# Kernel tuning notes

Measured on AMD Instinct MI355X. Metric: run time of the kernel, lower is better.

The kernel has to match this reference:

```python
import jax, jax.numpy as jnp
import numpy as np

B, S, H = 1, 1024, 1024   # batch, seq, hidden_size
E, I = 8, 2048            # num_local_experts, intermediate_size
JITTER_EPS = 0.01         # config.router_jitter_noise


def setup_inputs() -> dict:
    key = jax.random.key(0)
    ks = jax.random.split(key, 5)
    s_h = 1.0 / np.sqrt(H)
    s_i = 1.0 / np.sqrt(I)
    return {
        "hidden_states": jax.random.normal(ks[0], (B, S, H), jnp.float32),
        "gate_w": jax.random.normal(ks[1], (E, H), jnp.float32) * s_h,   # nn.Linear(H, E) weight
        "w1": jax.random.normal(ks[2], (E, I, H), jnp.float32) * s_h,    # per-expert Linear(H, I)
        "w2": jax.random.normal(ks[3], (E, H, I), jnp.float32) * s_i,    # per-expert Linear(I, H)
        "w3": jax.random.normal(ks[4], (E, I, H), jnp.float32) * s_h,    # per-expert Linear(H, I)
    }


def _sparse_mixer_top2(scores, jitter_eps):
    # masked_sampling_omp_inference (top_k=2, inference)
    vals, idx = jax.lax.top_k(scores, 2)                 # [T,2]
    neg_inf = jnp.array(-jnp.inf, scores.dtype)

    t1 = vals[:, :1]                                      # top-1 logit
    f1 = jnp.maximum(jnp.abs(scores), t1)                 # clamp(min=t1)
    m1 = (t1 - scores) / f1 > 2 * jitter_eps
    p1 = jax.nn.softmax(jnp.where(m1, neg_inf, scores), axis=-1)
    mult1 = jnp.take_along_axis(p1, idx[:, :1], axis=-1)

    t2 = vals[:, 1:2]                                     # top-2 logit
    f2 = jnp.maximum(jnp.abs(scores), t2)
    m2 = (t2 - scores) / f2 > 2 * jitter_eps
    rows = jnp.arange(scores.shape[0])[:, None]
    s2 = scores.at[rows, idx[:, :1]].set(neg_inf)         # scatter -inf at top-1 slot
    p2 = jax.nn.softmax(jnp.where(m2, neg_inf, s2), axis=-1)
    mult2 = jnp.take_along_axis(p2, idx[:, 1:2], axis=-1)

    return jnp.concatenate([mult1, mult2], axis=-1), idx  # [T,2], [T,2]


def reference(hidden_states, gate_w, w1, w2, w3):
    b, s, h = hidden_states.shape
    x = hidden_states.reshape(-1, h)                      # [T,H]
    T = x.shape[0]

    logits = x @ gate_w.T                                 # [T,E] router logits
    mult, sel = _sparse_mixer_top2(logits, JITTER_EPS)

    # dense [T,E] combine weights (zero for unselected experts);
    # mathematically identical to gather/expert-FFN/scatter-add with full capacity
    rows = jnp.arange(T)[:, None]
    dense_w = jnp.zeros((T, E), x.dtype).at[rows, sel].set(mult)

    h1 = jnp.einsum('th,eih->eti', x, w1)                 # [E,T,I]
    h3 = jnp.einsum('th,eih->eti', x, w3)                 # [E,T,I]
    act = jax.nn.silu(h1) * h3                            # SwiGLU
    y = jnp.einsum('eti,ehi->eth', act, w2)               # [E,T,H]
    out = jnp.einsum('eth,te->th', y, dense_w)            # weighted combine
    return out.reshape(b, s, h)
```

## Files before the change

kernel.cpp:

```cpp
#include <hip/hip_runtime.h>
#include <hip/hip_bf16.h>
#include <math.h>

#define TT 1024
#define HD 1024
#define NE 8
#define ID 2048
#define MAXSLOT 3072
constexpr float JEPS = 0.01f;

typedef __attribute__((ext_vector_type(8))) short bf16x8;
typedef __attribute__((ext_vector_type(4))) float f32x4;

__device__ __forceinline__ float silu_f(float v) {
    return v / (1.f + expf(-v));
}

__device__ __forceinline__ unsigned short f2bf(float f) {
    unsigned int u = __float_as_uint(f);
    u += 0x7FFF + ((u >> 16) & 1);
    return (unsigned short)(u >> 16);
}

__device__ __forceinline__ void st_bf4(unsigned short* p, float4 v) {
    __hip_bfloat162 lo = __float22bfloat162_rn(make_float2(v.x, v.y));
    __hip_bfloat162 hi = __float22bfloat162_rn(make_float2(v.z, v.w));
    union { __hip_bfloat162 h[2]; uint2 q; } pk;
    pk.h[0] = lo; pk.h[1] = hi;
    *(uint2*)p = pk.q;
}

__global__ __launch_bounds__(256) void gate_kernel(
    const float* __restrict__ x, const float* __restrict__ gw,
    int* __restrict__ sel, float* __restrict__ wgt, int* __restrict__ counts,
    unsigned short* __restrict__ xbf)
{
    int wave = threadIdx.x >> 6;
    int lane = threadIdx.x & 63;
    int t = blockIdx.x * 4 + wave;

    const float4* x4 = (const float4*)(x + (size_t)t * HD);
    const float4* g4 = (const float4*)gw;

    float acc[8] = {0.f,0.f,0.f,0.f,0.f,0.f,0.f,0.f};
    #pragma unroll
    for (int c = 0; c < 4; ++c) {
        float4 xv = x4[lane + c * 64];
        st_bf4(&xbf[(size_t)t * HD + (size_t)(lane + c * 64) * 4], xv);
        #pragma unroll
        for (int e = 0; e < 8; ++e) {
            float4 gv = g4[e * 256 + lane + c * 64];
            acc[e] += xv.x*gv.x + xv.y*gv.y + xv.z*gv.z + xv.w*gv.w;
        }
    }
    #pragma unroll
    for (int e = 0; e < 8; ++e) {
        float v = acc[e];
        #pragma unroll
        for (int off = 32; off > 0; off >>= 1) v += __shfl_xor(v, off, 64);
        acc[e] = v;
    }

    if (lane == 0) {
        float s[8];
        #pragma unroll
        for (int e = 0; e < 8; ++e) s[e] = acc[e];

        int i0 = 0; float t1 = s[0];
        #pragma unroll
        for (int e = 1; e < 8; ++e) { if (s[e] > t1) { t1 = s[e]; i0 = e; } }
        int i1 = -1; float t2 = -INFINITY;
        #pragma unroll
        for (int e = 0; e < 8; ++e) {
            if (e == i0) continue;
            if (s[e] > t2) { t2 = s[e]; i1 = e; }
        }

        float sum1 = 0.f;
        #pragma unroll
        for (int e = 0; e < 8; ++e) {
            if (e == i0) { sum1 += 1.f; continue; }
            float f = fmaxf(fabsf(s[e]), t1);
            bool masked = (t1 - s[e]) > 2.f * JEPS * f;
            if (!masked) sum1 += expf(s[e] - t1);
        }
        float w0 = 1.f / sum1;

        float sum2 = 0.f;
        #pragma unroll
        for (int e = 0; e < 8; ++e) {
            if (e == i0) continue;
            if (e == i1) { sum2 += 1.f; continue; }
            float f = fmaxf(fabsf(s[e]), t2);
            bool masked = (t2 - s[e]) > 2.f * JEPS * f;
            if (!masked) sum2 += expf(s[e] - t2);
        }
        float w1v = 1.f / sum2;

        sel[t * 2 + 0] = i0; sel[t * 2 + 1] = i1;
        wgt[t * 2 + 0] = w0; wgt[t * 2 + 1] = w1v;
        atomicAdd(&counts[i0], 1);
        atomicAdd(&counts[i1], 1);
    }
}

__global__ void offsets_kernel(const int* __restrict__ counts,
                               int* __restrict__ offs, int* __restrict__ cursor)
{
    int o = 0;
    for (int e = 0; e < NE; ++e) {
        offs[e] = o;
        cursor[e] = o;
        o += (counts[e] + 127) & ~127;
    }
}

__global__ __launch_bounds__(256) void scatter_kernel(
    const int* __restrict__ sel, const float* __restrict__ wgt,
    int* __restrict__ cursor, int* __restrict__ slot_token,
    float* __restrict__ slot_weight)
{
    int t = blockIdx.x * 256 + threadIdx.x;
    #pragma unroll
    for (int j = 0; j < 2; ++j) {
        int e = sel[t * 2 + j];
        int pos = atomicAdd(&cursor[e], 1);
        slot_token[pos] = t;
        slot_weight[pos] = wgt[t * 2 + j];
    }
}

__global__ __launch_bounds__(256) void ffn1_kernel(
    const unsigned short* __restrict__ xbf, const float* __restrict__ w1,
    const float* __restrict__ w3, const int* __restrict__ counts,
    const int* __restrict__ offs, const int* __restrict__ slot_token,
    unsigned short* __restrict__ act)
{
    int bid = blockIdx.x;
    int e = bid & 7;
    int r = bid >> 3;
    int it = r & 31, tt = r >> 5;
    int cnt = counts[e];
    if (tt * 128 >= cnt) return;
    int base = offs[e];

    __shared__ unsigned short Xs[2][128][40];
    __shared__ unsigned short W1s[2][64][40];
    __shared__ unsigned short W3s[2][64][40];

    int t = threadIdx.x;
    int xr = t >> 1, xs = (t & 1) * 16;
    int srow = tt * 128 + xr;
    int tok = (srow < cnt) ? slot_token[base + srow] : slot_token[base];
    const unsigned short* xptr = xbf + (size_t)tok * HD;
    int wrow = t >> 2, ws0 = t & 3;
    const float* w1ptr = w1 + ((size_t)e * ID + (size_t)it * 64 + wrow) * HD;
    const float* w3ptr = w3 + ((size_t)e * ID + (size_t)it * 64 + wrow) * HD;

    int wid = t >> 6, lane = t & 63;
    int wr = wid >> 1, wc = wid & 1;
    int fr = lane & 15, fg = lane >> 4;

    f32x4 a1[4][2], a3[4][2];
    #pragma unroll
    for (int m = 0; m < 4; ++m)
        #pragma unroll
        for (int n = 0; n < 2; ++n) {
            a1[m][n] = (f32x4){0.f, 0.f, 0.f, 0.f};
            a3[m][n] = (f32x4){0.f, 0.f, 0.f, 0.f};
        }

    uint4 pxa0, pxb0, pxa1, pxb1;
    float4 pw10[2], pw30[2], pw11[2], pw31[2];

#define F1_LOAD0(KT) do { \
    pxa0 = *(const uint4*)(xptr + (KT) + xs); \
    pxb0 = *(const uint4*)(xptr + (KT) + xs + 8); \
    pw10[0] = *(const float4*)(w1ptr + (KT) + ws0 * 4); \
    pw10[1] = *(const float4*)(w1ptr + (KT) + (ws0 + 4) * 4); \
    pw30[0] = *(const float4*)(w3ptr + (KT) + ws0 * 4); \
    pw30[1] = *(const float4*)(w3ptr + (KT) + (ws0 + 4) * 4); \
} while (0)
#define F1_LOAD1(KT) do { \
    pxa1 = *(const uint4*)(xptr + (KT) + xs); \
    pxb1 = *(const uint4*)(xptr + (KT) + xs + 8); \
    pw11[0] = *(const float4*)(w1ptr + (KT) + ws0 * 4); \
    pw11[1] = *(const float4*)(w1ptr + (KT) + (ws0 + 4) * 4); \
    pw31[0] = *(const float4*)(w3ptr + (KT) + ws0 * 4); \
    pw31[1] = *(const float4*)(w3ptr + (KT) + (ws0 + 4) * 4); \
} while (0)
#define F1_STORE0(B) do { \
    *(uint4*)&Xs[B][xr][xs] = pxa0; \
    *(uint4*)&Xs[B][xr][xs + 8] = pxb0; \
    st_bf4(&W1s[B][wrow][ws0 * 4], pw10[0]); \
    st_bf4(&W1s[B][wrow][(ws0 + 4) * 4], pw10[1]); \
    st_bf4(&W3s[B][wrow][ws0 * 4], pw30[0]); \
    st_bf4(&W3s[B][wrow][(ws0 + 4) * 4], pw30[1]); \
} while (0)
#define F1_STORE1(B) do { \
    *(uint4*)&Xs[B][xr][xs] = pxa1; \
    *(uint4*)&Xs[B][xr][xs + 8] = pxb1; \
    st_bf4(&W1s[B][wrow][ws0 * 4], pw11[0]); \
    st_bf4(&W1s[B][wrow][(ws0 + 4) * 4], pw11[1]); \
    st_bf4(&W3s[B][wrow][ws0 * 4], pw31[0]); \
    st_bf4(&W3s[B][wrow][(ws0 + 4) * 4], pw31[1]); \
} while (0)
#define F1_COMPUTE(B) do { \
    bf16x8 af[4], b1f[2], b3f[2]; \
    _Pragma("unroll") for (int m = 0; m < 4; ++m) \
        af[m] = *(const bf16x8*)&Xs[B][wr * 64 + m * 16 + fr][fg * 8]; \
    _Pragma("unroll") for (int n = 0; n < 2; ++n) { \
        b1f[n] = *(const bf16x8*)&W1s[B][wc * 32 + n * 16 + fr][fg * 8]; \
        b3f[n] = *(const bf16x8*)&W3s[B][wc * 32 + n * 16 + fr][fg * 8]; } \
    _Pragma("unroll") for (int m = 0; m < 4; ++m) \
        _Pragma("unroll") for (int n = 0; n < 2; ++n) { \
            a1[m][n] = __builtin_amdgcn_mfma_f32_16x16x32_bf16(af[m], b1f[n], a1[m][n], 0, 0, 0); \
            a3[m][n] = __builtin_amdgcn_mfma_f32_16x16x32_bf16(af[m], b3f[n], a3[m][n], 0, 0, 0); } \
} while (0)

    F1_LOAD0(0);
    F1_LOAD1(32);
    F1_STORE0(0);

    for (int kt = 0; kt < HD; kt += 64) {
        __syncthreads();
        if (kt + 64 < HD) F1_LOAD0(kt + 64);
        F1_COMPUTE(0);
        F1_STORE1(1);
        __syncthreads();
        if (kt + 96 < HD) F1_LOAD1(kt + 96);
        F1_COMPUTE(1);
        if (kt + 64 < HD) F1_STORE0(0);
    }
#undef F1_LOAD0
#undef F1_LOAD1
#undef F1_STORE0
#undef F1_STORE1
#undef F1_COMPUTE

    size_t rowbase = (size_t)(base + tt * 128);
    #pragma unroll
    for (int m = 0; m < 4; ++m)
        #pragma unroll
        for (int n = 0; n < 2; ++n)
            #pragma unroll
            for (int rr = 0; rr < 4; ++rr) {
                int lrow = wr * 64 + m * 16 + fg * 4 + rr;
                int col  = it * 64 + wc * 32 + n * 16 + fr;
                float v = silu_f(a1[m][n][rr]) * a3[m][n][rr];
                act[(rowbase + lrow) * ID + col] = f2bf(v);
            }
}

__global__ __launch_bounds__(256) void ffn2_kernel(
    const unsigned short* __restrict__ act, const float* __restrict__ w2,
    const int* __restrict__ counts, const int* __restrict__ offs,
    const int* __restrict__ slot_token, const float* __restrict__ slot_weight,
    float* __restrict__ out)
{
    int bid = blockIdx.x;
    int e = bid & 7;
    int r = bid >> 3;
    int ht = r & 15, tt = r >> 4;
    int cnt = counts[e];
    if (tt * 128 >= cnt) return;
    int base = offs[e];

    __shared__ unsigned short As[2][128][40];
    __shared__ unsigned short Bs[2][64][40];

    int t = threadIdx.x;
    int ar = t >> 1, as = (t & 1) * 16;
    const unsigned short* aptr = act + (size_t)(base + tt * 128 + ar) * ID;
    int wrow = t >> 2, ws0 = t & 3;
    const float* w2ptr = w2 + ((size_t)e * HD + (size_t)ht * 64 + wrow) * ID;

    int wid = t >> 6, lane = t & 63;
    int wr = wid >> 1, wc = wid & 1;
    int fr = lane & 15, fg = lane >> 4;

    f32x4 acc[4][2];
    #pragma unroll
    for (int m = 0; m < 4; ++m)
        #pragma unroll
        for (int n = 0; n < 2; ++n) acc[m][n] = (f32x4){0.f, 0.f, 0.f, 0.f};

    uint4 pa00, pa01, pa10, pa11;
    float4 pb0[2], pb1[2];

#define F2_LOAD0(KT) do { \
    pa00 = *(const uint4*)(aptr + (KT) + as); \
    pa01 = *(const uint4*)(aptr + (KT) + as + 8); \
    pb0[0] = *(const float4*)(w2ptr + (KT) + ws0 * 4); \
    pb0[1] = *(const float4*)(w2ptr + (KT) + (ws0 + 4) * 4); \
} while (0)
#define F2_LOAD1(KT) do { \
    pa10 = *(const uint4*)(aptr + (KT) + as); \
    pa11 = *(const uint4*)(aptr + (KT) + as + 8); \
    pb1[0] = *(const float4*)(w2ptr + (KT) + ws0 * 4); \
    pb1[1] = *(const float4*)(w2ptr + (KT) + (ws0 + 4) * 4); \
} while (0)
#define F2_STORE0(B) do { \
    *(uint4*)&As[B][ar][as] = pa00; \
    *(uint4*)&As[B][ar][as + 8] = pa01; \
    st_bf4(&Bs[B][wrow][ws0 * 4], pb0[0]); \
    st_bf4(&Bs[B][wrow][(ws0 + 4) * 4], pb0[1]); \
} while (0)
#define F2_STORE1(B) do { \
    *(uint4*)&As[B][ar][as] = pa10; \
    *(uint4*)&As[B][ar][as + 8] = pa11; \
    st_bf4(&Bs[B][wrow][ws0 * 4], pb1[0]); \
    st_bf4(&Bs[B][wrow][(ws0 + 4) * 4], pb1[1]); \
} while (0)
#define F2_COMPUTE(B) do { \
    bf16x8 af[4], bf[2]; \
    _Pragma("unroll") for (int m = 0; m < 4; ++m) \
        af[m] = *(const bf16x8*)&As[B][wr * 64 + m * 16 + fr][fg * 8]; \
    _Pragma("unroll") for (int n = 0; n < 2; ++n) \
        bf[n] = *(const bf16x8*)&Bs[B][wc * 32 + n * 16 + fr][fg * 8]; \
    _Pragma("unroll") for (int m = 0; m < 4; ++m) \
        _Pragma("unroll") for (int n = 0; n < 2; ++n) \
            acc[m][n] = __builtin_amdgcn_mfma_f32_16x16x32_bf16(af[m], bf[n], acc[m][n], 0, 0, 0); \
} while (0)

    F2_LOAD0(0);
    F2_LOAD1(32);
    F2_STORE0(0);

    for (int kt = 0; kt < ID; kt += 64) {
        __syncthreads();
        if (kt + 64 < ID) F2_LOAD0(kt + 64);
        F2_COMPUTE(0);
        F2_STORE1(1);
        __syncthreads();
        if (kt + 96 < ID) F2_LOAD1(kt + 96);
        F2_COMPUTE(1);
        if (kt + 64 < ID) F2_STORE0(0);
    }
#undef F2_LOAD0
#undef F2_LOAD1
#undef F2_STORE0
#undef F2_STORE1
#undef F2_COMPUTE

    #pragma unroll
    for (int m = 0; m < 4; ++m)
        #pragma unroll
        for (int rr = 0; rr < 4; ++rr) {
            int grow = tt * 128 + wr * 64 + m * 16 + fg * 4 + rr;
            if (grow < cnt) {
                int tok  = slot_token[base + grow];
                float wv = slot_weight[base + grow];
                float* orow = out + (size_t)tok * HD + ht * 64 + wc * 32;
                #pragma unroll
                for (int n = 0; n < 2; ++n)
                    atomicAdd(&orow[n * 16 + fr], wv * acc[m][n][rr]);
            }
        }
}

extern "C" void kernel_launch(void* const* d_in, const int* in_sizes, int n_in,
                              void* d_out, int out_size, void* d_ws, size_t ws_size,
                              hipStream_t stream)
{
    const float* x  = (const float*)d_in[0];
    const float* gw = (const float*)d_in[1];
    const float* w1 = (const float*)d_in[2];
    const float* w2 = (const float*)d_in[3];
    const float* w3 = (const float*)d_in[4];
    float* out = (float*)d_out;

    char* w = (char*)d_ws;
    int*   counts      = (int*)(w + 0);
    int*   offs        = (int*)(w + 64);
    int*   cursor      = (int*)(w + 128);
    int*   sel         = (int*)(w + 256);
    float* wgt         = (float*)(w + 256 + 8192);
    int*   slot_token  = (int*)(w + 16640);
    float* slot_weight = (float*)(w + 16640 + 4 * MAXSLOT);
    unsigned short* xbf = (unsigned short*)(w + 65536);
    unsigned short* act = (unsigned short*)(w + 65536 + 2 * TT * HD);

    hipMemsetAsync(counts, 0, 64, stream);
    hipMemsetAsync(d_out, 0, (size_t)TT * HD * sizeof(float), stream);

    gate_kernel<<<TT / 4, 256, 0, stream>>>(x, gw, sel, wgt, counts, xbf);
    offsets_kernel<<<1, 1, 0, stream>>>(counts, offs, cursor);
    scatter_kernel<<<TT / 256, 256, 0, stream>>>(sel, wgt, cursor, slot_token, slot_weight);
    ffn1_kernel<<<2048, 256, 0, stream>>>(xbf, w1, w3, counts, offs, slot_token, act);
    ffn2_kernel<<<1024, 256, 0, stream>>>(act, w2, counts, offs, slot_token, slot_weight, out);
}
```

Before: 152.5 us.

## Retile FFN kernels: smaller token tiles, 512-thread ffn1, single-stage K=32 pipeline

```diff
diff --git a/kernel.cpp b/kernel.cpp
--- a/kernel.cpp
+++ b/kernel.cpp
@@ -130,7 +130,7 @@
     }
 }
 
-__global__ __launch_bounds__(256) void ffn1_kernel(
+__global__ __launch_bounds__(512) void ffn1_kernel(
     const unsigned short* __restrict__ xbf, const float* __restrict__ w1,
     const float* __restrict__ w3, const int* __restrict__ counts,
     const int* __restrict__ offs, const int* __restrict__ slot_token,
@@ -139,7 +139,7 @@
     int bid = blockIdx.x;
     int e = bid & 7;
     int r = bid >> 3;
-    int it = r & 31, tt = r >> 5;
+    int tt = r & 7, it = r >> 3;
     int cnt = counts[e];
     if (tt * 128 >= cnt) return;
     int base = offs[e];
@@ -149,11 +149,11 @@
     __shared__ unsigned short W3s[2][64][40];
 
     int t = threadIdx.x;
-    int xr = t >> 1, xs = (t & 1) * 16;
+    int xr = t >> 2, xs = (t & 3) * 8;
     int srow = tt * 128 + xr;
     int tok = (srow < cnt) ? slot_token[base + srow] : slot_token[base];
     const unsigned short* xptr = xbf + (size_t)tok * HD;
-    int wrow = t >> 2, ws0 = t & 3;
+    int wrow = t >> 3, ws = (t & 7) * 4;
     const float* w1ptr = w1 + ((size_t)e * ID + (size_t)it * 64 + wrow) * HD;
     const float* w3ptr = w3 + ((size_t)e * ID + (size_t)it * 64 + wrow) * HD;
 
@@ -161,91 +161,64 @@
     int wr = wid >> 1, wc = wid & 1;
     int fr = lane & 15, fg = lane >> 4;
 
-    f32x4 a1[4][2], a3[4][2];
-    #pragma unroll
-    for (int m = 0; m < 4; ++m)
+    f32x4 a1[2][2], a3[2][2];
+    #pragma unroll
+    for (int m = 0; m < 2; ++m)
         #pragma unroll
         for (int n = 0; n < 2; ++n) {
             a1[m][n] = (f32x4){0.f, 0.f, 0.f, 0.f};
             a3[m][n] = (f32x4){0.f, 0.f, 0.f, 0.f};
         }
 
-    uint4 pxa0, pxb0, pxa1, pxb1;
-    float4 pw10[2], pw30[2], pw11[2], pw31[2];
-
-#define F1_LOAD0(KT) do { \
-    pxa0 = *(const uint4*)(xptr + (KT) + xs); \
-    pxb0 = *(const uint4*)(xptr + (KT) + xs + 8); \
-    pw10[0] = *(const float4*)(w1ptr + (KT) + ws0 * 4); \
-    pw10[1] = *(const float4*)(w1ptr + (KT) + (ws0 + 4) * 4); \
-    pw30[0] = *(const float4*)(w3ptr + (KT) + ws0 * 4); \
-    pw30[1] = *(const float4*)(w3ptr + (KT) + (ws0 + 4) * 4); \
-} while (0)
-#define F1_LOAD1(KT) do { \
-    pxa1 = *(const uint4*)(xptr + (KT) + xs); \
-    pxb1 = *(const uint4*)(xptr + (KT) + xs + 8); \
-    pw11[0] = *(const float4*)(w1ptr + (KT) + ws0 * 4); \
-    pw11[1] = *(const float4*)(w1ptr + (KT) + (ws0 + 4) * 4); \
-    pw31[0] = *(const float4*)(w3ptr + (KT) + ws0 * 4); \
-    pw31[1] = *(const float4*)(w3ptr + (KT) + (ws0 + 4) * 4); \
-} while (0)
-#define F1_STORE0(B) do { \
-    *(uint4*)&Xs[B][xr][xs] = pxa0; \
-    *(uint4*)&Xs[B][xr][xs + 8] = pxb0; \
-    st_bf4(&W1s[B][wrow][ws0 * 4], pw10[0]); \
-    st_bf4(&W1s[B][wrow][(ws0 + 4) * 4], pw10[1]); \
-    st_bf4(&W3s[B][wrow][ws0 * 4], pw30[0]); \
-    st_bf4(&W3s[B][wrow][(ws0 + 4) * 4], pw30[1]); \
-} while (0)
-#define F1_STORE1(B) do { \
-    *(uint4*)&Xs[B][xr][xs] = pxa1; \
-    *(uint4*)&Xs[B][xr][xs + 8] = pxb1; \
-    st_bf4(&W1s[B][wrow][ws0 * 4], pw11[0]); \
-    st_bf4(&W1s[B][wrow][(ws0 + 4) * 4], pw11[1]); \
-    st_bf4(&W3s[B][wrow][ws0 * 4], pw31[0]); \
-    st_bf4(&W3s[B][wrow][(ws0 + 4) * 4], pw31[1]); \
+    uint4 px;
+    float4 pw1v, pw3v;
+
+#define F1_LOAD(KT) do { \
+    px   = *(const uint4*)(xptr + (KT) + xs); \
+    pw1v = *(const float4*)(w1ptr + (KT) + ws); \
+    pw3v = *(const float4*)(w3ptr + (KT) + ws); \
+} while (0)
+#define F1_STORE(B) do { \
+    *(uint4*)&Xs[B][xr][xs] = px; \
+    st_bf4(&W1s[B][wrow][ws], pw1v); \
+    st_bf4(&W3s[B][wrow][ws], pw3v); \
 } while (0)
 #define F1_COMPUTE(B) do { \
-    bf16x8 af[4], b1f[2], b3f[2]; \
-    _Pragma("unroll") for (int m = 0; m < 4; ++m) \
-        af[m] = *(const bf16x8*)&Xs[B][wr * 64 + m * 16 + fr][fg * 8]; \
+    bf16x8 af[2], b1f[2], b3f[2]; \
+    _Pragma("unroll") for (int m = 0; m < 2; ++m) \
+        af[m] = *(const bf16x8*)&Xs[B][wr * 32 + m * 16 + fr][fg * 8]; \
     _Pragma("unroll") for (int n = 0; n < 2; ++n) { \
         b1f[n] = *(const bf16x8*)&W1s[B][wc * 32 + n * 16 + fr][fg * 8]; \
         b3f[n] = *(const bf16x8*)&W3s[B][wc * 32 + n * 16 + fr][fg * 8]; } \
-    _Pragma("unroll") for (int m = 0; m < 4; ++m) \
+    _Pragma("unroll") for (int m = 0; m < 2; ++m) \
         _Pragma("unroll") for (int n = 0; n < 2; ++n) { \
             a1[m][n] = __builtin_amdgcn_mfma_f32_16x16x32_bf16(af[m], b1f[n], a1[m][n], 0, 0, 0); \
             a3[m][n] = __builtin_amdgcn_mfma_f32_16x16x32_bf16(af[m], b3f[n], a3[m][n], 0, 0, 0); } \
 } while (0)
 
-    F1_LOAD0(0);
-    F1_LOAD1(32);
-    F1_STORE0(0);
-
-    for (int kt = 0; kt < HD; kt += 64) {
+    F1_LOAD(0);
+    F1_STORE(0);
+
+    for (int kt = 0; kt < HD; kt += 32) {
+        int cur = (kt >> 5) & 1;
         __syncthreads();
-        if (kt + 64 < HD) F1_LOAD0(kt + 64);
-        F1_COMPUTE(0);
-        F1_STORE1(1);
-        __syncthreads();
-        if (kt + 96 < HD) F1_LOAD1(kt + 96);
-        F1_COMPUTE(1);
-        if (kt + 64 < HD) F1_STORE0(0);
-    }
-#undef F1_LOAD0
-#undef F1_LOAD1
-#undef F1_STORE0
-#undef F1_STORE1
+        bool more = (kt + 32) < HD;
+        if (more) F1_LOAD(kt + 32);
+        F1_COMPUTE(cur);
+        if (more) F1_STORE(cur ^ 1);
+    }
+#undef F1_LOAD
+#undef F1_STORE
 #undef F1_COMPUTE
 
     size_t rowbase = (size_t)(base + tt * 128);
     #pragma unroll
-    for (int m = 0; m < 4; ++m)
+    for (int m = 0; m < 2; ++m)
         #pragma unroll
         for (int n = 0; n < 2; ++n)
             #pragma unroll
             for (int rr = 0; rr < 4; ++rr) {
-                int lrow = wr * 64 + m * 16 + fg * 4 + rr;
+                int lrow = wr * 32 + m * 16 + fg * 4 + rr;
                 int col  = it * 64 + wc * 32 + n * 16 + fr;
                 float v = silu_f(a1[m][n][rr]) * a3[m][n][rr];
                 act[(rowbase + lrow) * ID + col] = f2bf(v);
@@ -261,64 +234,60 @@
     int bid = blockIdx.x;
     int e = bid & 7;
     int r = bid >> 3;
-    int ht = r & 15, tt = r >> 4;
+    int tt = r & 15, ht = r >> 4;
     int cnt = counts[e];
-    if (tt * 128 >= cnt) return;
+    if (tt * 64 >= cnt) return;
     int base = offs[e];
 
-    __shared__ unsigned short As[2][128][40];
+    __shared__ unsigned short As[2][64][40];
     __shared__ unsigned short Bs[2][64][40];
 
     int t = threadIdx.x;
-    int ar = t >> 1, as = (t & 1) * 16;
-    const unsigned short* aptr = act + (size_t)(base + tt * 128 + ar) * ID;
-    int wrow = t >> 2, ws0 = t & 3;
+    int ar = t >> 2, as = (t & 3) * 8;
+    const unsigned short* aptr = act + (size_t)(base + tt * 64 + ar) * ID;
+    int wrow = t >> 2, ws = (t & 3) * 8;
     const float* w2ptr = w2 + ((size_t)e * HD + (size_t)ht * 64 + wrow) * ID;
 
     int wid = t >> 6, lane = t & 63;
     int wr = wid >> 1, wc = wid & 1;
     int fr = lane & 15, fg = lane >> 4;
 
-    f32x4 acc[4][2];
-    #pragma unroll
-    for (int m = 0; m < 4; ++m)
+    f32x4 acc[2][2];
+    #pragma unroll
+    for (int m = 0; m < 2; ++m)
         #pragma unroll
         for (int n = 0; n < 2; ++n) acc[m][n] = (f32x4){0.f, 0.f, 0.f, 0.f};
 
-    uint4 pa00, pa01, pa10, pa11;
+    uint4 pa0, pa1;
     float4 pb0[2], pb1[2];
 
 #define F2_LOAD0(KT) do { \
-    pa00 = *(const uint4*)(aptr + (KT) + as); \
-    pa01 = *(const uint4*)(aptr + (KT) + as + 8); \
-    pb0[0] = *(const float4*)(w2ptr + (KT) + ws0 * 4); \
-    pb0[1] = *(const float4*)(w2ptr + (KT) + (ws0 + 4) * 4); \
+    pa0 = *(const uint4*)(aptr + (KT) + as); \
+    pb0[0] = *(const float4*)(w2ptr + (KT) + ws); \
+    pb0[1] = *(const float4*)(w2ptr + (KT) + ws + 4); \
 } while (0)
 #define F2_LOAD1(KT) do { \
-    pa10 = *(const uint4*)(aptr + (KT) + as); \
-    pa11 = *(const uint4*)(aptr + (KT) + as + 8); \
-    pb1[0] = *(const float4*)(w2ptr + (KT) + ws0 * 4); \
-    pb1[1] = *(const float4*)(w2ptr + (KT) + (ws0 + 4) * 4); \
+    pa1 = *(const uint4*)(aptr + (KT) + as); \
+    pb1[0] = *(const float4*)(w2ptr + (KT) + ws); \
+    pb1[1] = *(const float4*)(w2ptr + (KT) + ws + 4); \
 } while (0)
 #define F2_STORE0(B) do { \
-    *(uint4*)&As[B][ar][as] = pa00; \
-    *(uint4*)&As[B][ar][as + 8] = pa01; \
-    st_bf4(&Bs[B][wrow][ws0 * 4], pb0[0]); \
-    st_bf4(&Bs[B][wrow][(ws0 + 4) * 4], pb0[1]); \
+    *(uint4*)&As[B][ar][as] = pa0; \
+    st_bf4(&Bs[B][wrow][ws], pb0[0]); \
+    st_bf4(&Bs[B][wrow][ws + 4], pb0[1]); \
 } while (0)
 #define F2_STORE1(B) do { \
-    *(uint4*)&As[B][ar][as] = pa10; \
-    *(uint4*)&As[B][ar][as + 8] = pa11; \
-    st_bf4(&Bs[B][wrow][ws0 * 4], pb1[0]); \
-    st_bf4(&Bs[B][wrow][(ws0 + 4) * 4], pb1[1]); \
+    *(uint4*)&As[B][ar][as] = pa1; \
+    st_bf4(&Bs[B][wrow][ws], pb1[0]); \
+    st_bf4(&Bs[B][wrow][ws + 4], pb1[1]); \
 } while (0)
 #define F2_COMPUTE(B) do { \
-    bf16x8 af[4], bf[2]; \
-    _Pragma("unroll") for (int m = 0; m < 4; ++m) \
-        af[m] = *(const bf16x8*)&As[B][wr * 64 + m * 16 + fr][fg * 8]; \
+    bf16x8 af[2], bf[2]; \
+    _Pragma("unroll") for (int m = 0; m < 2; ++m) \
+        af[m] = *(const bf16x8*)&As[B][wr * 32 + m * 16 + fr][fg * 8]; \
     _Pragma("unroll") for (int n = 0; n < 2; ++n) \
         bf[n] = *(const bf16x8*)&Bs[B][wc * 32 + n * 16 + fr][fg * 8]; \
-    _Pragma("unroll") for (int m = 0; m < 4; ++m) \
+    _Pragma("unroll") for (int m = 0; m < 2; ++m) \
         _Pragma("unroll") for (int n = 0; n < 2; ++n) \
             acc[m][n] = __builtin_amdgcn_mfma_f32_16x16x32_bf16(af[m], bf[n], acc[m][n], 0, 0, 0); \
 } while (0)
@@ -344,10 +313,10 @@
 #undef F2_COMPUTE
 
     #pragma unroll
-    for (int m = 0; m < 4; ++m)
+    for (int m = 0; m < 2; ++m)
         #pragma unroll
         for (int rr = 0; rr < 4; ++rr) {
-            int grow = tt * 128 + wr * 64 + m * 16 + fg * 4 + rr;
+            int grow = tt * 64 + wr * 32 + m * 16 + fg * 4 + rr;
             if (grow < cnt) {
                 int tok  = slot_token[base + grow];
                 float wv = slot_weight[base + grow];
@@ -387,6 +356,6 @@
     gate_kernel<<<TT / 4, 256, 0, stream>>>(x, gw, sel, wgt, counts, xbf);
     offsets_kernel<<<1, 1, 0, stream>>>(counts, offs, cursor);
     scatter_kernel<<<TT / 256, 256, 0, stream>>>(sel, wgt, cursor, slot_token, slot_weight);
-    ffn1_kernel<<<2048, 256, 0, stream>>>(xbf, w1, w3, counts, offs, slot_token, act);
-    ffn2_kernel<<<1024, 256, 0, stream>>>(act, w2, counts, offs, slot_token, slot_weight, out);
-}
+    ffn1_kernel<<<2048, 512, 0, stream>>>(xbf, w1, w3, counts, offs, slot_token, act);
+    ffn2_kernel<<<2048, 256, 0, stream>>>(act, w2, counts, offs, slot_token, slot_weight, out);
+}
```

New measurement: 162.7 us. 6.7% more time.
